# Kernel optimization log

Hardware: AMD Instinct MI355X
Metric: run time of the kernel (lower is better)

Reference implementation:

```python
import jax, jax.numpy as jnp
import numpy as np

C, H2, E, SQ, SK, HW = 256, 256, 512, 2048, 64, 256

def setup_inputs() -> dict:
    key = jax.random.key(0)
    ks = jax.random.split(key, 12)
    s = 0.05
    return {
        "Z": jax.random.normal(ks[0], (C, HW, HW), jnp.float32),
        "Q": jax.random.normal(ks[1], (SQ, 3), jnp.float32),
        "q_z": jax.random.normal(ks[2], (SQ, C), jnp.float32),
        "r": jax.random.uniform(ks[3], (SQ, SK, 2), jnp.float32) * (HW - 2),
        "w1": jax.random.normal(ks[4], (H2, 2), jnp.float32) * s,
        "b1": jnp.zeros((H2,), jnp.float32),
        "w2": jax.random.normal(ks[5], (H2, 3), jnp.float32) * s,
        "b2": jnp.zeros((H2,), jnp.float32),
        "in_proj_w": jax.random.normal(ks[6], (3 * E, E), jnp.float32) * s,
        "in_proj_b": jnp.zeros((3 * E,), jnp.float32),
        "out_proj_w": jax.random.normal(ks[7], (E, E), jnp.float32) * s,
        "out_proj_b": jnp.zeros((E,), jnp.float32),
        "num_heads": 8,
    }

def bilinear_interpolation_3d(Z, x, y):
    # Z: [c, H, W]; x, y: [N] float coords. Faithful to torch: .int() trunc (coords >= 0)
    c = Z.shape[0]
    x1 = x.astype(jnp.int32)
    y1 = y.astype(jnp.int32)
    x2 = x1 + 1
    y2 = y1 + 1
    Q11 = Z[:, x1, y1]  # [c, N]
    Q12 = Z[:, x1, y2]
    Q21 = Z[:, x2, y1]
    Q22 = Z[:, x2, y2]
    dx = x - x1
    dy = y - y1
    R1 = Q11 * (1 - dx) + Q21 * dx
    R2 = Q12 * (1 - dx) + Q22 * dx
    interp = R1 * (1 - dy) + R2 * dy  # [c, N]
    # faithful to the original: raw row-major reshape (NOT a transpose)
    return jnp.reshape(interp, (-1, c))

def reference(Z, Q, q_z, r, w1, b1, w2, b2, in_proj_w, in_proj_b, out_proj_w, out_proj_b, num_heads):
    size_q, size_k, _ = r.shape
    qr = r.reshape(-1, 2)
    Zr = bilinear_interpolation_3d(Z, qr[:, 0], qr[:, 1])
    Zr = Zr.reshape(size_q, size_k, -1)  # [sq, sk, c]
    r_proj = r @ w1.T + b1               # [sq, sk, h2]
    key = jnp.concatenate([Zr, r_proj], axis=2)  # [sq, sk, E]
    value = key
    q_proj = Q @ w2.T + b2               # [sq, h2]
    query = jnp.concatenate([q_z, q_proj], axis=1)  # [sq, E]
    E_ = query.shape[1]
    hd = E_ // num_heads
    # torch MultiheadAttention in-projection
    ql = query @ in_proj_w[:E_].T + in_proj_b[:E_]              # [sq, E]
    kl = key @ in_proj_w[E_:2 * E_].T + in_proj_b[E_:2 * E_]    # [sq, sk, E]
    vl = value @ in_proj_w[2 * E_:].T + in_proj_b[2 * E_:]
    qh = ql.reshape(size_q, num_heads, hd)
    kh = kl.reshape(size_q, size_k, num_heads, hd)
    vh = vl.reshape(size_q, size_k, num_heads, hd)
    scores = jnp.einsum('bhd,bkhd->bhk', qh, kh) / jnp.sqrt(jnp.asarray(hd, qh.dtype))
    attn = jax.nn.softmax(scores, axis=-1)  # [sq, h, sk]
    out = jnp.einsum('bhk,bkhd->bhd', attn, vh).reshape(size_q, E_)
    out = out @ out_proj_w.T + out_proj_b
    return jnp.concatenate([q_z, out], axis=1)  # [sq, c + E]
```

## Files before the change

### kernel.cpp

```cpp
#include <hip/hip_runtime.h>


typedef _Float16 half8 __attribute__((ext_vector_type(8)));
typedef _Float16 half4v __attribute__((ext_vector_type(4)));
typedef float f32x4 __attribute__((ext_vector_type(4)));

#define O_WQT   0u
#define O_WKT   262144u
#define O_WVT   524288u
#define O_WO    786432u
#define O_QRY   1048576u
#define O_WCT   2097152u
#define O_MT    4194304u
#define O_U     6291456u
#define O_G     14680064u
#define O_ZT    23068672u
#define O_ZR    39845888u
#define O_F32   73400320u

__global__ __launch_bounds__(256) void k_prep(
    const float* __restrict__ ipw, const float* __restrict__ opw,
    const float* __restrict__ q_z, const float* __restrict__ Qm,
    const float* __restrict__ w2, const float* __restrict__ b2,
    const float* __restrict__ ipb, const float* __restrict__ opb,
    _Float16* __restrict__ wsh, float* __restrict__ bu, float* __restrict__ b_eff)
{
    int idx = blockIdx.x * 256 + threadIdx.x;
    if (idx < 1048576) {
        int q = idx >> 9, j = idx & 511;
        float v;
        if (j < 256) v = q_z[q * 256 + j];
        else {
            int m = j - 256;
            v = Qm[q * 3] * w2[m * 3] + Qm[q * 3 + 1] * w2[m * 3 + 1]
              + Qm[q * 3 + 2] * w2[m * 3 + 2] + b2[m];
        }
        wsh[O_QRY + idx] = (_Float16)v;
    } else if (idx < 1310720) {
        int e0 = idx - 1048576;
        int i = e0 >> 9, e = e0 & 511;
        wsh[O_WQT + e0] = (_Float16)ipw[(size_t)e * 512 + i];
    } else if (idx < 1572864) {
        int e0 = idx - 1310720;
        int d = e0 & 63, j = (e0 >> 6) & 511, h = e0 >> 15;
        wsh[O_WKT + e0] = (_Float16)(0.125f * ipw[(size_t)(512 + (h << 6) + d) * 512 + j]);
    } else if (idx < 1835008) {
        int e0 = idx - 1572864;
        int d = e0 & 63, j = (e0 >> 6) & 511, h = e0 >> 15;
        wsh[O_WVT + e0] = (_Float16)ipw[(size_t)(1024 + (h << 6) + d) * 512 + j];
    } else if (idx < 2097152) {
        int e0 = idx - 1835008;
        wsh[O_WO + e0] = (_Float16)opw[e0];
    } else if (idx < 2101248) {
        int c = idx - 2097152;
        int h = c >> 9, j = c & 511;
        float s = 0.f;
        for (int d = 0; d < 64; ++d)
            s += ipb[512 + (h << 6) + d] * ipw[(size_t)(512 + (h << 6) + d) * 512 + j];
        bu[c] = 0.125f * s;
    } else if (idx < 2101760) {
        int e = idx - 2101248;
        float s = opb[e];
        const float* worow = opw + (size_t)e * 512;
        for (int n = 0; n < 512; ++n) s += ipb[1024 + n] * worow[n];
        b_eff[e] = s;
    }
}

__global__ __launch_bounds__(256) void k_zt(
    const float* __restrict__ Z, _Float16* __restrict__ Zt)
{
    __shared__ float sT[256][67];
    int x = blockIdx.x, yt = blockIdx.y * 64;
    int t = threadIdx.x;
#pragma unroll
    for (int i = 0; i < 16; ++i) {
        int c = i * 16 + (t >> 4), y = (t & 15) * 4;
        float4 v = *(const float4*)(Z + (size_t)c * 65536 + x * 256 + yt + y);
        sT[c][y] = v.x; sT[c][y + 1] = v.y; sT[c][y + 2] = v.z; sT[c][y + 3] = v.w;
    }
    __syncthreads();
    _Float16* outb = Zt + ((size_t)(x * 256 + yt)) * 256 + t;
#pragma unroll 8
    for (int y = 0; y < 64; ++y)
        outb[(size_t)y * 256] = (_Float16)sT[t][y];
}

__global__ __launch_bounds__(256, 4) void k_passA(
    const _Float16* __restrict__ Zt, const float* __restrict__ r,
    _Float16* __restrict__ Zr)
{
    __shared__ float sT[256][33];
    int b = blockIdx.x;
    int t = threadIdx.x, w = t >> 6, l = t & 63;
    const float2* r2 = (const float2*)r;

#pragma unroll 2
    for (int i = 0; i < 8; ++i) {
        int ptl = w * 8 + i;
        float2 rv = r2[b * 32 + ptl];
        int x1 = (int)rv.x, y1 = (int)rv.y;
        float dx = rv.x - (float)x1, dy = rv.y - (float)y1;
        float w11 = (1.f - dx) * (1.f - dy), w21 = dx * (1.f - dy);
        float w12 = (1.f - dx) * dy,         w22 = dx * dy;
        const _Float16* base = Zt + ((size_t)(x1 * 256 + y1)) * 256;
#pragma unroll
        for (int cg = 0; cg < 4; ++cg) {
            int c = (cg << 6) + l;
            float z11 = (float)base[c];
            float z12 = (float)base[256 + c];
            float z21 = (float)base[65536 + c];
            float z22 = (float)base[65536 + 256 + c];
            sT[c][ptl] = w11 * z11 + w21 * z21 + w12 * z12 + w22 * z22;
        }
    }
    __syncthreads();
    int ch0 = t >> 2, colc = (t & 3) * 8;
#pragma unroll
    for (int g = 0; g < 4; ++g) {
        int ch = g * 64 + ch0;
        half8 o;
#pragma unroll
        for (int j = 0; j < 8; ++j) o[j] = (_Float16)sT[ch][colc + j];
        *(half8*)(Zr + (size_t)ch * 131072 + b * 32 + colc) = o;
    }
}

__global__ __launch_bounds__(256) void k_small(
    const _Float16* __restrict__ A, const _Float16* __restrict__ BT,
    _Float16* __restrict__ C, int outT)
{
    __shared__ __align__(16) _Float16 sA[64][72];
    int rb = blockIdx.x, h = blockIdx.y;
    int t = threadIdx.x, w = t >> 6, l = t & 63;
    const _Float16* A0 = A + (size_t)rb * 64 * 512 + h * 64;
    const _Float16* B0 = BT + (size_t)h * 512 * 64;
#pragma unroll
    for (int i = 0; i < 2; ++i) {
        int g = t + i * 256;
        int row = g >> 3, colg = (g & 7) * 8;
        *(half8*)&sA[row][colg] = *(const half8*)(A0 + (size_t)row * 512 + colg);
    }
    __syncthreads();
    f32x4 acc[4][8] = {};
    int arow = l & 15, kg = (l >> 4) << 3;
#pragma unroll
    for (int kk = 0; kk < 64; kk += 32) {
        half8 a[4], bb[8];
#pragma unroll
        for (int mt = 0; mt < 4; ++mt) a[mt] = *(const half8*)&sA[mt * 16 + arow][kk + kg];
#pragma unroll
        for (int nt = 0; nt < 8; ++nt) {
            int col = (w << 7) + nt * 16 + arow;
            bb[nt] = *(const half8*)(B0 + (size_t)col * 64 + kk + kg);
        }
#pragma unroll
        for (int mt = 0; mt < 4; ++mt)
#pragma unroll
            for (int nt = 0; nt < 8; ++nt)
                acc[mt][nt] = __builtin_amdgcn_mfma_f32_16x16x32_f16(a[mt], bb[nt], acc[mt][nt], 0, 0, 0);
    }
    if (outT) {
#pragma unroll
        for (int mt = 0; mt < 4; ++mt)
#pragma unroll
            for (int nt = 0; nt < 8; ++nt) {
                int col = (h << 9) + (w << 7) + nt * 16 + arow;
                int row0 = rb * 64 + mt * 16 + ((l >> 4) << 2);
                half4v v4;
#pragma unroll
                for (int v = 0; v < 4; ++v) v4[v] = (_Float16)acc[mt][nt][v];
                *(half4v*)(C + (size_t)col * 512 + row0) = v4;
            }
    } else {
        _Float16* C0 = C + (size_t)rb * 64 * 4096 + h * 512;
#pragma unroll
        for (int mt = 0; mt < 4; ++mt)
#pragma unroll
            for (int nt = 0; nt < 8; ++nt)
#pragma unroll
                for (int v = 0; v < 4; ++v) {
                    int row = mt * 16 + ((l >> 4) << 2) + v;
                    int col = (w << 7) + nt * 16 + arow;
                    C0[(size_t)row * 4096 + col] = (_Float16)acc[mt][nt][v];
                }
    }
}

__global__ __launch_bounds__(256) void k_gemmU(
    const _Float16* __restrict__ A, const _Float16* __restrict__ B,
    const float* __restrict__ bu, _Float16* __restrict__ U)
{
    __shared__ __align__(16) _Float16 sA[64][520];
    int q0 = blockIdx.x * 64;
    int t = threadIdx.x, w = t >> 6, l = t & 63;
    int colb = blockIdx.y * 256 + w * 64;
    const _Float16* Ab = A + (size_t)q0 * 512;
#pragma unroll
    for (int i = 0; i < 16; ++i) {
        int e = i * 2048 + t * 8;
        *(half8*)&sA[e >> 9][e & 511] = *(const half8*)(Ab + e);
    }
    __syncthreads();
    f32x4 acc[4][4] = {};
    int arow = l & 15, kg = (l >> 4) << 3;
#pragma unroll 2
    for (int kk = 0; kk < 512; kk += 32) {
        half8 a[4], bb[4];
#pragma unroll
        for (int mt = 0; mt < 4; ++mt) a[mt] = *(const half8*)&sA[mt * 16 + arow][kk + kg];
#pragma unroll
        for (int nt = 0; nt < 4; ++nt)
            bb[nt] = *(const half8*)(B + (size_t)(colb + nt * 16 + arow) * 512 + kk + kg);
#pragma unroll
        for (int mt = 0; mt < 4; ++mt)
#pragma unroll
            for (int nt = 0; nt < 4; ++nt)
                acc[mt][nt] = __builtin_amdgcn_mfma_f32_16x16x32_f16(a[mt], bb[nt], acc[mt][nt], 0, 0, 0);
    }
#pragma unroll
    for (int mt = 0; mt < 4; ++mt)
#pragma unroll
        for (int nt = 0; nt < 4; ++nt)
#pragma unroll
            for (int v = 0; v < 4; ++v) {
                int row = q0 + mt * 16 + ((l >> 4) << 2) + v;
                int col = colb + nt * 16 + arow;
                U[(size_t)row * 4096 + col] = (_Float16)(acc[mt][nt][v] + bu[col]);
            }
}

__global__ __launch_bounds__(512, 4) void k_main(
    const _Float16* __restrict__ Zr, const float* __restrict__ r,
    const float* __restrict__ w1, const float* __restrict__ b1,
    const _Float16* __restrict__ U, _Float16* __restrict__ G)
{
    __shared__ __align__(16) _Float16 sKey[64][520];
    __shared__ __align__(16) _Float16 sU[8][520];
    __shared__ float sP[512];

    int q = blockIdx.x;
    int t = threadIdx.x, w = t >> 6, l = t & 63;
    int ch = q >> 3, s8 = q & 7;

    const _Float16* src = Zr + ((size_t)ch * 2048 + s8 * 256) * 64;
#pragma unroll
    for (int i = 0; i < 4; ++i) {
        int e = i * 4096 + t * 8;
        *(half8*)&sKey[e >> 8][e & 255] = *(const half8*)(src + e);
    }
    {
        int e = t * 8;
        *(half8*)&sU[e >> 9][e & 511] = *(const half8*)(U + (size_t)q * 4096 + e);
    }
    {
        int m = t & 255, half = t >> 8;
        float w10 = w1[2 * m], w11 = w1[2 * m + 1], b1m = b1[m];
        const float2* r2q = (const float2*)r + (size_t)q * 64;
#pragma unroll 8
        for (int i = 0; i < 32; ++i) {
            int k = half * 32 + i;
            float2 rv = r2q[k];
            sKey[k][256 + m] = (_Float16)(rv.x * w10 + rv.y * w11 + b1m);
        }
    }
    __syncthreads();

    if (w < 4) {
        f32x4 acc = {};
        int arow = l & 15, kg = (l >> 4) << 3;
        const _Float16* ar = &sKey[w * 16 + arow][kg];
        const _Float16* br = &sU[l & 7][kg];
#pragma unroll 4
        for (int kk = 0; kk < 512; kk += 32)
            acc = __builtin_amdgcn_mfma_f32_16x16x32_f16(
                *(const half8*)(ar + kk), *(const half8*)(br + kk), acc, 0, 0, 0);
        if ((l & 15) < 8) {
            int h = l & 15, krow0 = w * 16 + ((l >> 4) << 2);
#pragma unroll
            for (int v = 0; v < 4; ++v) sP[(h << 6) + krow0 + v] = acc[v];
        }
    }
    __syncthreads();

    {
        float v = sP[t];
        float mx = v;
#pragma unroll
        for (int mm = 1; mm < 64; mm <<= 1) mx = fmaxf(mx, __shfl_xor(mx, mm, 64));
        float e = __expf(v - mx);
        float sm = e;
#pragma unroll
        for (int mm = 1; mm < 64; mm <<= 1) sm += __shfl_xor(sm, mm, 64);
        sP[t] = e / sm;
    }
    __syncthreads();

    {
        const float* attn = &sP[w << 6];
        float g8[8] = {};
#pragma unroll 8
        for (int k = 0; k < 64; ++k) {
            half8 kv = *(const half8*)&sKey[k][l * 8];
            float a = attn[k];
#pragma unroll
            for (int x = 0; x < 8; ++x) g8[x] += a * (float)kv[x];
        }
        half8 go;
#pragma unroll
        for (int x = 0; x < 8; ++x) go[x] = (_Float16)g8[x];
        *(half8*)(G + (size_t)q * 4096 + t * 8) = go;
    }
}

__global__ __launch_bounds__(256) void k_final(
    const _Float16* __restrict__ G, const _Float16* __restrict__ Mt,
    const float* __restrict__ b_eff, const float* __restrict__ qz,
    float* __restrict__ out)
{
    __shared__ __align__(16) _Float16 sA[64][520];
    int rb = blockIdx.x, cb = blockIdx.y;
    int q0 = rb * 64;
    int t = threadIdx.x, w = t >> 6, l = t & 63;

    if (cb == 0) {
#pragma unroll
        for (int i = 0; i < 16; ++i) {
            int idx4 = i * 256 + t;
            int row = idx4 >> 6, c = (idx4 & 63) << 2;
            *(float4*)&out[(size_t)(q0 + row) * 768 + c] =
                *(const float4*)&qz[(size_t)(q0 + row) * 256 + c];
        }
    }

    f32x4 acc[4] = {};
    int arow = l & 15, kg = (l >> 4) << 3;
    int ecol = cb * 64 + w * 16 + arow;
    const _Float16* Brow = Mt + (size_t)ecol * 4096;
    for (int c = 0; c < 8; ++c) {
#pragma unroll
        for (int i = 0; i < 16; ++i) {
            int e = i * 2048 + t * 8;
            *(half8*)&sA[e >> 9][e & 511] = *(const half8*)(G + (size_t)(q0 + (e >> 9)) * 4096 + c * 512 + (e & 511));
        }
        __syncthreads();
#pragma unroll 4
        for (int kk = 0; kk < 512; kk += 32) {
            half8 bb = *(const half8*)(Brow + c * 512 + kk + kg);
#pragma unroll
            for (int mt = 0; mt < 4; ++mt) {
                half8 a = *(const half8*)&sA[mt * 16 + arow][kk + kg];
                acc[mt] = __builtin_amdgcn_mfma_f32_16x16x32_f16(a, bb, acc[mt], 0, 0, 0);
            }
        }
        __syncthreads();
    }
#pragma unroll
    for (int mt = 0; mt < 4; ++mt)
#pragma unroll
        for (int v = 0; v < 4; ++v) {
            int row = q0 + mt * 16 + ((l >> 4) << 2) + v;
            out[(size_t)row * 768 + 256 + ecol] = acc[mt][v] + b_eff[ecol];
        }
}

extern "C" void kernel_launch(void* const* d_in, const int* in_sizes, int n_in,
                              void* d_out, int out_size, void* d_ws, size_t ws_size,
                              hipStream_t stream) {
    const float* Z          = (const float*)d_in[0];
    const float* Qm         = (const float*)d_in[1];
    const float* q_z        = (const float*)d_in[2];
    const float* r          = (const float*)d_in[3];
    const float* w1         = (const float*)d_in[4];
    const float* b1         = (const float*)d_in[5];
    const float* w2         = (const float*)d_in[6];
    const float* b2         = (const float*)d_in[7];
    const float* in_proj_w  = (const float*)d_in[8];
    const float* in_proj_b  = (const float*)d_in[9];
    const float* out_proj_w = (const float*)d_in[10];
    const float* out_proj_b = (const float*)d_in[11];
    float* out = (float*)d_out;

    _Float16* wsh = (_Float16*)d_ws;
    _Float16* wqT   = wsh + O_WQT;
    _Float16* wkT   = wsh + O_WKT;
    _Float16* wvT   = wsh + O_WVT;
    _Float16* wo    = wsh + O_WO;
    _Float16* query = wsh + O_QRY;
    _Float16* WcT   = wsh + O_WCT;
    _Float16* Mt    = wsh + O_MT;
    _Float16* U     = wsh + O_U;
    _Float16* G     = wsh + O_G;
    _Float16* Zt    = wsh + O_ZT;
    _Float16* Zr    = wsh + O_ZR;
    float*    bu    = (float*)(wsh + O_F32);
    float*    b_eff = bu + 4096;

    k_prep<<<8210, 256, 0, stream>>>(in_proj_w, out_proj_w, q_z, Qm, w2, b2,
                                     in_proj_b, out_proj_b, wsh, bu, b_eff);
    k_zt<<<dim3(256, 4), 256, 0, stream>>>(Z, Zt);
    k_small<<<dim3(8, 8), 256, 0, stream>>>(wqT, wkT, WcT, 1);
    k_small<<<dim3(8, 8), 256, 0, stream>>>(wo, wvT, Mt, 0);
    k_gemmU<<<dim3(32, 16), 256, 0, stream>>>(query, WcT, bu, U);
    k_passA<<<4096, 256, 0, stream>>>(Zt, r, Zr);
    k_main<<<2048, 512, 0, stream>>>(Zr, r, w1, b1, U, G);
    k_final<<<dim3(32, 8), 256, 0, stream>>>(G, Mt, b_eff, q_z, out);
}
```

Before: 321.4 us.

## Tile weight transposes, vectorize gathers, use MFMA for attention-weighted sum

Moves the strided per-element weight transposes out of k_prep into a new LDS-tiled transpose kernel with half8 stores. The bilinear gather now loads two channels per half2 access. In k_main, the per-thread scalar attention-weighted reduction becomes an MFMA over an fp16 attention tile in LDS, and the occupancy hint drops from 4 to 2. k_final computes 2 column tiles per wave over half as many blocks to reuse A fragments, and one k_small output path goes back to scalar stores. The goal is less uncoalesced traffic and fewer scalar FMAs, at the cost of an extra launch and fp16 rounding of the attention weights.

Result: faster. 312.7 us (-2.7%).

```diff
diff --git a/kernel.cpp b/kernel.cpp
--- a/kernel.cpp
+++ b/kernel.cpp
@@ -2,7 +2,7 @@
 
 
 typedef _Float16 half8 __attribute__((ext_vector_type(8)));
-typedef _Float16 half4v __attribute__((ext_vector_type(4)));
+typedef _Float16 half2v __attribute__((ext_vector_type(2)));
 typedef float f32x4 __attribute__((ext_vector_type(4)));
 
 #define O_WQT   0u
@@ -38,28 +38,16 @@
         wsh[O_QRY + idx] = (_Float16)v;
     } else if (idx < 1310720) {
         int e0 = idx - 1048576;
-        int i = e0 >> 9, e = e0 & 511;
-        wsh[O_WQT + e0] = (_Float16)ipw[(size_t)e * 512 + i];
-    } else if (idx < 1572864) {
-        int e0 = idx - 1310720;
-        int d = e0 & 63, j = (e0 >> 6) & 511, h = e0 >> 15;
-        wsh[O_WKT + e0] = (_Float16)(0.125f * ipw[(size_t)(512 + (h << 6) + d) * 512 + j]);
-    } else if (idx < 1835008) {
-        int e0 = idx - 1572864;
-        int d = e0 & 63, j = (e0 >> 6) & 511, h = e0 >> 15;
-        wsh[O_WVT + e0] = (_Float16)ipw[(size_t)(1024 + (h << 6) + d) * 512 + j];
-    } else if (idx < 2097152) {
-        int e0 = idx - 1835008;
         wsh[O_WO + e0] = (_Float16)opw[e0];
-    } else if (idx < 2101248) {
-        int c = idx - 2097152;
+    } else if (idx < 1314816) {
+        int c = idx - 1310720;
         int h = c >> 9, j = c & 511;
         float s = 0.f;
         for (int d = 0; d < 64; ++d)
             s += ipb[512 + (h << 6) + d] * ipw[(size_t)(512 + (h << 6) + d) * 512 + j];
         bu[c] = 0.125f * s;
-    } else if (idx < 2101760) {
-        int e = idx - 2101248;
+    } else if (idx < 1315328) {
+        int e = idx - 1314816;
         float s = opb[e];
         const float* worow = opw + (size_t)e * 512;
         for (int n = 0; n < 512; ++n) s += ipb[1024 + n] * worow[n];
@@ -67,6 +55,41 @@
     }
 }
 
+__global__ __launch_bounds__(256) void k_tw(
+    const float* __restrict__ ipw, _Float16* __restrict__ wsh)
+{
+    __shared__ float sT[64][65];
+    int bx = blockIdx.x;
+    int sec = bx >> 6, tile = bx & 63;
+    int t = threadIdx.x;
+    int th = tile >> 3, tl = tile & 7;
+    int row0, col0;
+    if (sec == 0) { row0 = tl * 64;             col0 = th * 64; }
+    else          { row0 = 512 * sec + th * 64; col0 = tl * 64; }
+    const float* src = ipw + (size_t)row0 * 512 + col0;
+#pragma unroll
+    for (int i = 0; i < 4; ++i) {
+        int rr = i * 16 + (t >> 4), cc = (t & 15) * 4;
+        float4 v = *(const float4*)(src + (size_t)rr * 512 + cc);
+        sT[rr][cc] = v.x; sT[rr][cc + 1] = v.y; sT[rr][cc + 2] = v.z; sT[rr][cc + 3] = v.w;
+    }
+    __syncthreads();
+    float scale = (sec == 1) ? 0.125f : 1.0f;
+#pragma unroll
+    for (int it = 0; it < 2; ++it) {
+        int g = t + it * 256;
+        int a = g >> 3, b8 = (g & 7) * 8;
+        half8 o;
+#pragma unroll
+        for (int j = 0; j < 8; ++j) o[j] = (_Float16)(scale * sT[b8 + j][a]);
+        size_t dst;
+        if (sec == 0)      dst = O_WQT + (size_t)(th * 64 + a) * 512 + tl * 64 + b8;
+        else if (sec == 1) dst = O_WKT + (size_t)th * 32768 + (size_t)(tl * 64 + a) * 64 + b8;
+        else               dst = O_WVT + (size_t)th * 32768 + (size_t)(tl * 64 + a) * 64 + b8;
+        *(half8*)(wsh + dst) = o;
+    }
+}
+
 __global__ __launch_bounds__(256) void k_zt(
     const float* __restrict__ Z, _Float16* __restrict__ Zt)
 {
@@ -94,7 +117,6 @@
     int b = blockIdx.x;
     int t = threadIdx.x, w = t >> 6, l = t & 63;
     const float2* r2 = (const float2*)r;
-
 #pragma unroll 2
     for (int i = 0; i < 8; ++i) {
         int ptl = w * 8 + i;
@@ -105,13 +127,16 @@
         float w12 = (1.f - dx) * dy,         w22 = dx * dy;
         const _Float16* base = Zt + ((size_t)(x1 * 256 + y1)) * 256;
 #pragma unroll
-        for (int cg = 0; cg < 4; ++cg) {
-            int c = (cg << 6) + l;
-            float z11 = (float)base[c];
-            float z12 = (float)base[256 + c];
-            float z21 = (float)base[65536 + c];
-            float z22 = (float)base[65536 + 256 + c];
-            sT[c][ptl] = w11 * z11 + w21 * z21 + w12 * z12 + w22 * z22;
+        for (int cg = 0; cg < 2; ++cg) {
+            int c = cg * 128 + l * 2;
+            half2v z11 = *(const half2v*)(base + c);
+            half2v z12 = *(const half2v*)(base + 256 + c);
+            half2v z21 = *(const half2v*)(base + 65536 + c);
+            half2v z22 = *(const half2v*)(base + 65536 + 256 + c);
+            sT[c][ptl]     = w11 * (float)z11[0] + w21 * (float)z21[0]
+                           + w12 * (float)z12[0] + w22 * (float)z22[0];
+            sT[c + 1][ptl] = w11 * (float)z11[1] + w21 * (float)z21[1]
+                           + w12 * (float)z12[1] + w22 * (float)z22[1];
         }
     }
     __syncthreads();
@@ -167,10 +192,9 @@
             for (int nt = 0; nt < 8; ++nt) {
                 int col = (h << 9) + (w << 7) + nt * 16 + arow;
                 int row0 = rb * 64 + mt * 16 + ((l >> 4) << 2);
-                half4v v4;
-#pragma unroll
-                for (int v = 0; v < 4; ++v) v4[v] = (_Float16)acc[mt][nt][v];
-                *(half4v*)(C + (size_t)col * 512 + row0) = v4;
+#pragma unroll
+                for (int v = 0; v < 4; ++v)
+                    C[(size_t)col * 512 + row0 + v] = (_Float16)acc[mt][nt][v];
             }
     } else {
         _Float16* C0 = C + (size_t)rb * 64 * 4096 + h * 512;
@@ -230,7 +254,7 @@
             }
 }
 
-__global__ __launch_bounds__(512, 4) void k_main(
+__global__ __launch_bounds__(512, 2) void k_main(
     const _Float16* __restrict__ Zr, const float* __restrict__ r,
     const float* __restrict__ w1, const float* __restrict__ b1,
     const _Float16* __restrict__ U, _Float16* __restrict__ G)
@@ -238,10 +262,13 @@
     __shared__ __align__(16) _Float16 sKey[64][520];
     __shared__ __align__(16) _Float16 sU[8][520];
     __shared__ float sP[512];
+    __shared__ __align__(16) _Float16 sA16[16][72];
 
     int q = blockIdx.x;
     int t = threadIdx.x, w = t >> 6, l = t & 63;
     int ch = q >> 3, s8 = q & 7;
+
+    for (int i = t; i < 576; i += 512) ((unsigned*)sA16)[i] = 0u;
 
     const _Float16* src = Zr + ((size_t)ch * 2048 + s8 * 256) * 64;
 #pragma unroll
@@ -292,24 +319,42 @@
         float sm = e;
 #pragma unroll
         for (int mm = 1; mm < 64; mm <<= 1) sm += __shfl_xor(sm, mm, 64);
-        sP[t] = e / sm;
+        sA16[w][l] = (_Float16)(e / sm);
     }
     __syncthreads();
 
     {
-        const float* attn = &sP[w << 6];
-        float g8[8] = {};
-#pragma unroll 8
-        for (int k = 0; k < 64; ++k) {
-            half8 kv = *(const half8*)&sKey[k][l * 8];
-            float a = attn[k];
-#pragma unroll
-            for (int x = 0; x < 8; ++x) g8[x] += a * (float)kv[x];
-        }
-        half8 go;
-#pragma unroll
-        for (int x = 0; x < 8; ++x) go[x] = (_Float16)g8[x];
-        *(half8*)(G + (size_t)q * 4096 + t * 8) = go;
+        f32x4 acc[4] = {};
+        int arow = l & 15, kq = (l >> 4) << 3;
+        half8 a0 = *(const half8*)&sA16[arow][kq];
+        half8 a1 = *(const half8*)&sA16[arow][32 + kq];
+#pragma unroll
+        for (int nt = 0; nt < 4; ++nt) {
+            int n0 = (w << 6) + (nt << 4);
+            half8 b0, b1f;
+#pragma unroll
+            for (int jj = 0; jj < 8; ++jj) b0[jj] = sKey[kq + jj][n0 + arow];
+            acc[nt] = __builtin_amdgcn_mfma_f32_16x16x32_f16(a0, b0, acc[nt], 0, 0, 0);
+#pragma unroll
+            for (int jj = 0; jj < 8; ++jj) b1f[jj] = sKey[32 + kq + jj][n0 + arow];
+            acc[nt] = __builtin_amdgcn_mfma_f32_16x16x32_f16(a1, b1f, acc[nt], 0, 0, 0);
+        }
+        if (l < 32) {
+            int rgrp = (l >> 4) << 2;
+#pragma unroll
+            for (int nt = 0; nt < 4; ++nt) {
+                int n0 = (w << 6) + (nt << 4);
+#pragma unroll
+                for (int v = 0; v < 4; ++v)
+                    sU[rgrp + v][n0 + arow] = (_Float16)acc[nt][v];
+            }
+        }
+    }
+    __syncthreads();
+
+    {
+        int c = t * 8;
+        *(half8*)(G + (size_t)q * 4096 + c) = *(const half8*)&sU[c >> 9][c & 511];
     }
 }
 
@@ -333,24 +378,29 @@
         }
     }
 
-    f32x4 acc[4] = {};
+    f32x4 acc[4][2] = {};
     int arow = l & 15, kg = (l >> 4) << 3;
-    int ecol = cb * 64 + w * 16 + arow;
-    const _Float16* Brow = Mt + (size_t)ecol * 4096;
+    int e0 = cb * 128 + (w << 5);
     for (int c = 0; c < 8; ++c) {
 #pragma unroll
         for (int i = 0; i < 16; ++i) {
             int e = i * 2048 + t * 8;
-            *(half8*)&sA[e >> 9][e & 511] = *(const half8*)(G + (size_t)(q0 + (e >> 9)) * 4096 + c * 512 + (e & 511));
+            *(half8*)&sA[e >> 9][e & 511] =
+                *(const half8*)(G + (size_t)(q0 + (e >> 9)) * 4096 + c * 512 + (e & 511));
         }
         __syncthreads();
 #pragma unroll 4
         for (int kk = 0; kk < 512; kk += 32) {
-            half8 bb = *(const half8*)(Brow + c * 512 + kk + kg);
+            half8 a[4], bb[2];
+#pragma unroll
+            for (int nt = 0; nt < 2; ++nt)
+                bb[nt] = *(const half8*)(Mt + (size_t)(e0 + nt * 16 + arow) * 4096 + c * 512 + kk + kg);
 #pragma unroll
             for (int mt = 0; mt < 4; ++mt) {
-                half8 a = *(const half8*)&sA[mt * 16 + arow][kk + kg];
-                acc[mt] = __builtin_amdgcn_mfma_f32_16x16x32_f16(a, bb, acc[mt], 0, 0, 0);
+                a[mt] = *(const half8*)&sA[mt * 16 + arow][kk + kg];
+#pragma unroll
+                for (int nt = 0; nt < 2; ++nt)
+                    acc[mt][nt] = __builtin_amdgcn_mfma_f32_16x16x32_f16(a[mt], bb[nt], acc[mt][nt], 0, 0, 0);
             }
         }
         __syncthreads();
@@ -358,10 +408,13 @@
 #pragma unroll
     for (int mt = 0; mt < 4; ++mt)
 #pragma unroll
-        for (int v = 0; v < 4; ++v) {
-            int row = q0 + mt * 16 + ((l >> 4) << 2) + v;
-            out[(size_t)row * 768 + 256 + ecol] = acc[mt][v] + b_eff[ecol];
-        }
+        for (int nt = 0; nt < 2; ++nt)
+#pragma unroll
+            for (int v = 0; v < 4; ++v) {
+                int row = q0 + mt * 16 + ((l >> 4) << 2) + v;
+                int ecol = e0 + nt * 16 + arow;
+                out[(size_t)row * 768 + 256 + ecol] = acc[mt][nt][v] + b_eff[ecol];
+            }
 }
 
 extern "C" void kernel_launch(void* const* d_in, const int* in_sizes, int n_in,
@@ -396,13 +449,14 @@
     float*    bu    = (float*)(wsh + O_F32);
     float*    b_eff = bu + 4096;
 
-    k_prep<<<8210, 256, 0, stream>>>(in_proj_w, out_proj_w, q_z, Qm, w2, b2,
+    k_prep<<<5138, 256, 0, stream>>>(in_proj_w, out_proj_w, q_z, Qm, w2, b2,
                                      in_proj_b, out_proj_b, wsh, bu, b_eff);
+    k_tw<<<192, 256, 0, stream>>>(in_proj_w, wsh);
     k_zt<<<dim3(256, 4), 256, 0, stream>>>(Z, Zt);
     k_small<<<dim3(8, 8), 256, 0, stream>>>(wqT, wkT, WcT, 1);
     k_small<<<dim3(8, 8), 256, 0, stream>>>(wo, wvT, Mt, 0);
     k_gemmU<<<dim3(32, 16), 256, 0, stream>>>(query, WcT, bu, U);
     k_passA<<<4096, 256, 0, stream>>>(Zt, r, Zr);
     k_main<<<2048, 512, 0, stream>>>(Zr, r, w1, b1, U, G);
-    k_final<<<dim3(32, 8), 256, 0, stream>>>(G, Mt, b_eff, q_z, out);
-}
+    k_final<<<dim3(32, 4), 256, 0, stream>>>(G, Mt, b_eff, q_z, out);
+}
```
